# Kernel optimization log

Measured on AMD Instinct MI355X. Metric: run time of the kernel, lower is better.

Reference implementation:

```python
import jax, jax.numpy as jnp
import numpy as np

RNN = 2048
NZ = 64
IN = 69  # 54 dofs + 15 actions


def gru_cell(x, h, w_ih, w_hh, b_ih, b_hh):
    gi = x @ w_ih.T + b_ih
    gh = h @ w_hh.T + b_hh
    i_r, i_z, i_n = jnp.split(gi, 3, axis=-1)
    h_r, h_z, h_n = jnp.split(gh, 3, axis=-1)
    r = jax.nn.sigmoid(i_r + h_r)
    z = jax.nn.sigmoid(i_z + h_z)
    n = jnp.tanh(i_n + r * h_n)
    return (1.0 - z) * n + z * h


def setup_inputs() -> dict:
    key = jax.random.key(0)
    ks = jax.random.split(key, 24)
    s = 0.02
    d = {
        'encoder_inputs': jax.random.normal(ks[0], (256, 49, IN), jnp.float32),
        'decoder_inputs': jax.random.normal(ks[1], (256, 25, IN), jnp.float32),
        'eps': jax.random.normal(ks[2], (256, NZ), jnp.float32),
        'fc0_w': jax.random.normal(ks[3], (RNN, 2 * IN), jnp.float32) * s,
        'fc0_b': jnp.zeros((RNN,), jnp.float32),
        'fc1_w': jax.random.normal(ks[4], (RNN, NZ + IN), jnp.float32) * s,
        'fc1_b': jnp.zeros((RNN,), jnp.float32),
        'fc2_w': jax.random.normal(ks[5], (IN, RNN), jnp.float32) * s,
        'fc2_b': jnp.zeros((IN,), jnp.float32),
        'mu_w': jax.random.normal(ks[6], (NZ, RNN), jnp.float32) * s,
        'mu_b': jnp.zeros((NZ,), jnp.float32),
        'sigma_w': jax.random.normal(ks[7], (NZ, RNN), jnp.float32) * s,
        'sigma_b': jnp.zeros((NZ,), jnp.float32),
        'c1_wih': jax.random.normal(ks[8], (3 * RNN, RNN), jnp.float32) * s,
        'c1_whh': jax.random.normal(ks[9], (3 * RNN, RNN), jnp.float32) * s,
        'c1_bih': jnp.zeros((3 * RNN,), jnp.float32),
        'c1_bhh': jnp.zeros((3 * RNN,), jnp.float32),
        'c2_wih': jax.random.normal(ks[10], (3 * RNN, IN), jnp.float32) * s,
        'c2_whh': jax.random.normal(ks[11], (3 * RNN, RNN), jnp.float32) * s,
        'c2_bih': jnp.zeros((3 * RNN,), jnp.float32),
        'c2_bhh': jnp.zeros((3 * RNN,), jnp.float32),
    }
    return d


def reference(encoder_inputs, decoder_inputs, eps, fc0_w, fc0_b, fc1_w, fc1_b, fc2_w, fc2_b,
              mu_w, mu_b, sigma_w, sigma_b, c1_wih, c1_whh, c1_bih, c1_bhh,
              c2_wih, c2_whh, c2_bih, c2_bhh):
    B = encoder_inputs.shape[0]
    enc_t = jnp.transpose(encoder_inputs, (1, 0, 2))  # [S-1, B, IN]
    dec_t = jnp.transpose(decoder_inputs, (1, 0, 2))  # [T, B, IN]
    # encoder step inputs: cat(enc[i], enc[i+1]); last step pairs with dec[0]
    nxt = jnp.concatenate([enc_t[1:], dec_t[:1]], axis=0)
    pairs = jnp.concatenate([enc_t, nxt], axis=-1)  # [S-1, B, 2*IN]
    x = pairs @ fc0_w.T + fc0_b  # fc0, [S-1, B, RNN]
    # precompute input-to-hidden GEMMs for all encoder steps
    gi_all = x @ c1_wih.T + c1_bih  # [S-1, B, 3*RNN]

    def enc_step(h, gi):
        gh = h @ c1_whh.T + c1_bhh
        i_r, i_z, i_n = jnp.split(gi, 3, axis=-1)
        h_r, h_z, h_n = jnp.split(gh, 3, axis=-1)
        r = jax.nn.sigmoid(i_r + h_r)
        z = jax.nn.sigmoid(i_z + h_z)
        n = jnp.tanh(i_n + r * h_n)
        return (1.0 - z) * n + z * h, None

    h0 = jnp.zeros((B, RNN), encoder_inputs.dtype)
    state, _ = jax.lax.scan(enc_step, h0, gi_all)

    z_mu = state @ mu_w.T + mu_b
    z_logvar = state @ sigma_w.T + sigma_b
    z = z_mu + eps * jnp.exp(0.5 * z_logvar)

    dec0 = dec_t[0]  # [B, IN]
    state = jnp.concatenate([z, dec0], axis=-1) @ fc1_w.T + fc1_b

    def dec_step(carry, _):
        h, inp = carry
        h = gru_cell(inp, h, c2_wih, c2_whh, c2_bih, c2_bhh)
        out = inp + (h @ fc2_w.T + fc2_b)  # residual feedback (eval: no dropout)
        return (h, out), out

    T = dec_t.shape[0]
    _, ys = jax.lax.scan(dec_step, (state, dec0), None, length=T)  # [T, B, IN]
    outputs = jnp.transpose(ys, (1, 0, 2))
    return outputs, z_mu, z_logvar
```

## Files before the change

kernel.cpp:

```cpp
#include <hip/hip_runtime.h>
#include <stdint.h>

#define B_    256
#define SE    49
#define TD    25
#define INDIM 69
#define RNN   2048
#define NZ    64
#define G3    6144

typedef __attribute__((ext_vector_type(8))) short short8_t;
typedef __attribute__((ext_vector_type(4))) float f32x4;
typedef unsigned short u16;

__device__ __forceinline__ float b2f(u16 u) {
  union { unsigned u; float f; } c; c.u = ((unsigned)u) << 16; return c.f;
}
__device__ __forceinline__ u16 f2b(float f) {
  union { float f; unsigned u; } c; c.f = f;
  unsigned u = c.u;
  return (u16)((u + 0x7FFFu + ((u >> 16) & 1u)) >> 16);
}
__device__ __forceinline__ float sigm(float x) { return 1.f / (1.f + __expf(-x)); }

__device__ __forceinline__ int rmap(int R) {
  int bn = R / 96, rem = R % 96;
  int nw = rem / 48, g = (rem % 48) / 16, jj = rem % 16;
  return g * RNN + bn * 32 + nw * 16 + jj;
}

__global__ void k_reorder(const float* __restrict__ src, u16* __restrict__ dst, int K, int Kp) {
  int total = G3 * Kp;
  for (int i = blockIdx.x * blockDim.x + threadIdx.x; i < total; i += gridDim.x * blockDim.x) {
    int R = i / Kp, c = i % Kp;
    dst[i] = (c < K) ? f2b(src[(size_t)rmap(R) * K + c]) : (u16)0;
  }
}

__global__ void k_fc0T(const float* __restrict__ fc0w, u16* __restrict__ dst) {
  int total = 256 * RNN;
  for (int i = blockIdx.x * blockDim.x + threadIdx.x; i < total; i += gridDim.x * blockDim.x) {
    int r = i >> 11, k = i & (RNN - 1);
    dst[i] = (r < 2 * INDIM) ? f2b(fc0w[(size_t)k * (2 * INDIM) + r]) : (u16)0;
  }
}

__global__ void k_fc2T(const float* __restrict__ fc2w, u16* __restrict__ dst) {
  int total = 96 * RNN;
  for (int i = blockIdx.x * blockDim.x + threadIdx.x; i < total; i += gridDim.x * blockDim.x) {
    int r = i >> 11, k = i & (RNN - 1);
    dst[i] = (r < INDIM) ? f2b(fc2w[(size_t)r * RNN + k]) : (u16)0;
  }
}

__global__ void k_pairs(const float* __restrict__ enc, const float* __restrict__ dec,
                        u16* __restrict__ pairs) {
  int total = SE * B_ * 256;
  for (int i = blockIdx.x * blockDim.x + threadIdx.x; i < total; i += gridDim.x * blockDim.x) {
    int c = i & 255, rb = i >> 8;
    int b = rb & 255, t = rb >> 8;
    float v = 0.f;
    if (c < INDIM) v = enc[((size_t)b * SE + t) * INDIM + c];
    else if (c < 2 * INDIM) {
      int cc = c - INDIM;
      v = (t < SE - 1) ? enc[((size_t)b * SE + t + 1) * INDIM + cc]
                       : dec[(size_t)b * TD * INDIM + cc];
    }
    pairs[i] = f2b(v);
  }
}

__global__ void k_msT(const float* __restrict__ muw, const float* __restrict__ sgw,
                      float* __restrict__ dst) {
  int total = RNN * 128;
  for (int i = blockIdx.x * blockDim.x + threadIdx.x; i < total; i += gridDim.x * blockDim.x) {
    int k = i >> 7, n = i & 127;
    dst[i] = (n < NZ) ? muw[(size_t)n * RNN + k] : sgw[(size_t)(n - NZ) * RNN + k];
  }
}

__global__ void k_fc1T(const float* __restrict__ w, float* __restrict__ dst) {
  int total = (NZ + INDIM) * RNN;
  for (int i = blockIdx.x * blockDim.x + threadIdx.x; i < total; i += gridDim.x * blockDim.x) {
    int k = i >> 11, n = i & (RNN - 1);
    dst[i] = w[(size_t)n * (NZ + INDIM) + k];
  }
}

__global__ void k_bias(const float* __restrict__ c1wih, const float* __restrict__ fc0b,
                       const float* __restrict__ c1bih, const float* __restrict__ c1bhh,
                       const float* __restrict__ c2wih, const float* __restrict__ fc2b,
                       const float* __restrict__ c2bih, const float* __restrict__ c2bhh,
                       float* __restrict__ ebi, float* __restrict__ ebh,
                       float* __restrict__ dbi0, float* __restrict__ dbi1, float* __restrict__ dbh) {
  int R = blockIdx.x;
  int orig = rmap(R);
  float s = 0.f;
  for (int k = threadIdx.x; k < RNN; k += 256) s += c1wih[(size_t)orig * RNN + k] * fc0b[k];
  __shared__ float red[256];
  red[threadIdx.x] = s; __syncthreads();
  for (int st = 128; st > 0; st >>= 1) {
    if (threadIdx.x < st) red[threadIdx.x] += red[threadIdx.x + st];
    __syncthreads();
  }
  if (threadIdx.x == 0) {
    float k3 = 0.f;
    for (int o = 0; o < INDIM; ++o) k3 += c2wih[(size_t)orig * INDIM + o] * fc2b[o];
    ebi[R] = red[0] + c1bih[orig];
    ebh[R] = c1bhh[orig];
    float d0 = c2bih[orig];
    dbi0[R] = d0;
    dbi1[R] = d0 + k3;
    dbh[R] = c2bhh[orig];
  }
}

__global__ void k_init(float* __restrict__ hf, u16* __restrict__ hbf, float* __restrict__ fbuf,
                       float* __restrict__ omu, float* __restrict__ olv) {
  int i = blockIdx.x * blockDim.x + threadIdx.x;
  if (i < B_ * RNN) { hf[i] = 0.f; hbf[i] = 0; }
  if (i < 3 * B_ * 96) fbuf[i] = 0.f;
  if (i < B_ * NZ) { omu[i] = 0.f; olv[i] = 0.f; }
}

__global__ __launch_bounds__(256) void gemm_bt(
    const u16* __restrict__ A, const u16* __restrict__ W,
    u16* __restrict__ Cb, int N, int K)
{
  constexpr int BM = 128, BN = 128, BK = 64, LDK = BK + 8;
  __shared__ u16 sA[BM * LDK];
  __shared__ u16 sW[BN * LDK];
  const int ntn = N / BN;
  const int bm = blockIdx.x / ntn, bn = blockIdx.x % ntn;
  const int tid = threadIdx.x, lane = tid & 63, wave = tid >> 6;
  const int wr = wave >> 1, wc = wave & 1;
  f32x4 acc[4][4];
#pragma unroll
// ... 24 lines not shown
      for (int m = 0; m < 4; ++m)
#pragma unroll
        for (int n = 0; n < 4; ++n)
          acc[m][n] = __builtin_amdgcn_mfma_f32_16x16x32_bf16(fa[m], fb[n], acc[m][n], 0, 0, 0);
    }
    __syncthreads();
  }
  const int crow = (lane >> 4) * 4, ccol = lane & 15;
#pragma unroll
  for (int n = 0; n < 4; ++n) {
    int col = bn * BN + wc * 64 + n * 16 + ccol;
#pragma unroll
    for (int m = 0; m < 4; ++m)
#pragma unroll
      for (int r = 0; r < 4; ++r) {
        int rowi = bm * BM + wr * 64 + m * 16 + crow + r;
        Cb[(size_t)rowi * N + col] = f2b(acc[m][n][r]);
      }
  }
}

struct Args {
  const u16 *pairs, *Wenc, *whh1, *whh2, *wih2, *fc2T;
  const float *ebi, *ebh, *dbi0, *dbi1, *dbh;
  const float *eps, *dec, *fc1_b, *fc2_b;
  const float *mswT, *fc1T, *mu_b, *sg_b;
  float* hf;
  u16*   hbf;
  float* fbuf;
  float* inp;
  u16*   inpbf;
  float* fc1x;
  float *out, *out_mu, *out_lv;
};

__device__ __forceinline__ void stage_gh(short8_t (&ra)[4], short8_t (&rw)[6],
    const u16* __restrict__ A, const u16* __restrict__ W,
    int rowA0, int rowW0, int k0, int tid) {
#pragma unroll
  for (int p = 0; p < 4; ++p) {
    int s = tid + p * 512, r = s >> 5, c = s & 31;
    ra[p] = *(const short8_t*)&A[(size_t)(rowA0 + r) * RNN + k0 + c * 8];
  }
#pragma unroll
  for (int p = 0; p < 6; ++p) {
    int s = tid + p * 512, r = s >> 5, c = s & 31;
    rw[p] = *(const short8_t*)&W[(size_t)(rowW0 + r) * RNN + k0 + c * 8];
  }
}

__device__ __forceinline__ void write_AW(char* sA, char* sW,
    short8_t (&ra)[4], short8_t (&rw)[6], int tid) {
#pragma unroll
  for (int p = 0; p < 4; ++p) {
    int s = tid + p * 512, r = s >> 5, c = s & 31;
    *(short8_t*)&sA[r * 512 + ((c ^ ((r & 7) << 2)) * 16)] = ra[p];
  }
#pragma unroll
  for (int p = 0; p < 6; ++p) {
    int s = tid + p * 512, r = s >> 5, c = s & 31;
    *(short8_t*)&sW[r * 512 + ((c ^ ((r & 7) << 2)) * 16)] = rw[p];
  }
}

__device__ __forceinline__ void compute2(const char* sA, const char* sW,
    f32x4 (&aR)[4], f32x4 (&aZ)[4], f32x4 (&aN)[4], int kg, int nw, int lane) {
#pragma unroll
  for (int s = 0; s < 2; ++s) {
    const int L = kg * 8 + s * 4 + (lane >> 4);
    short8_t fa[4], fbv[3];
#pragma unroll
    for (int m = 0; m < 4; ++m) {
      int r = m * 16 + (lane & 15);
      fa[m] = *(const short8_t*)&sA[r * 512 + ((L ^ ((r & 7) << 2)) * 16)];
    }
#pragma unroll
    for (int g = 0; g < 3; ++g) {
      int r = nw * 48 + g * 16 + (lane & 15);
      fbv[g] = *(const short8_t*)&sW[r * 512 + ((L ^ ((r & 7) << 2)) * 16)];
    }
#pragma unroll
    for (int m = 0; m < 4; ++m) {
      aR[m] = __builtin_amdgcn_mfma_f32_16x16x32_bf16(fa[m], fbv[0], aR[m], 0, 0, 0);
      aZ[m] = __builtin_amdgcn_mfma_f32_16x16x32_bf16(fa[m], fbv[1], aZ[m], 0, 0, 0);
      aN[m] = __builtin_amdgcn_mfma_f32_16x16x32_bf16(fa[m], fbv[2], aN[m], 0, 0, 0);
    }
  }
}

__device__ __forceinline__ void reduce_and_gate(
    f32x4 (&aR)[4], f32x4 (&aZ)[4], f32x4 (&aNI)[4], f32x4 (&aNH)[4],
    char* smem, int tid, int bm, int bn,
    const float* __restrict__ bi, const float* __restrict__ bh,
    const float* __restrict__ hfold, float* __restrict__ hfnew, u16* __restrict__ hbnew) {
  const int lane = tid & 63, wid = tid >> 6;
  auto wr16 = [&](int slots, int w) {
#pragma unroll
    for (int m = 0; m < 4; ++m) {
      *(f32x4*)&smem[(((0 * 4 + m) * slots + w) * 64 + lane) * 16] = aR[m];
      *(f32x4*)&smem[(((1 * 4 + m) * slots + w) * 64 + lane) * 16] = aZ[m];
      *(f32x4*)&smem[(((2 * 4 + m) * slots + w) * 64 + lane) * 16] = aNI[m];
      *(f32x4*)&smem[(((3 * 4 + m) * slots + w) * 64 + lane) * 16] = aNH[m];
    }
  };
  auto add16 = [&](int slots, int w) {
#pragma unroll
    for (int m = 0; m < 4; ++m) {
      aR[m]  += *(const f32x4*)&smem[(((0 * 4 + m) * slots + w) * 64 + lane) * 16];
      aZ[m]  += *(const f32x4*)&smem[(((1 * 4 + m) * slots + w) * 64 + lane) * 16];
      aNI[m] += *(const f32x4*)&smem[(((2 * 4 + m) * slots + w) * 64 + lane) * 16];
      aNH[m] += *(const f32x4*)&smem[(((3 * 4 + m) * slots + w) * 64 + lane) * 16];
// ... 10 lines not shown
    add16(2, wid);
    const int nw = wid, jj = lane & 15;
    const int Rb = bn * 96 + nw * 48;
    const float biR = bi[Rb + jj],      bhR = bh[Rb + jj];
    const float biZ = bi[Rb + 16 + jj], bhZ = bh[Rb + 16 + jj];
    const float biN = bi[Rb + 32 + jj], bhN = bh[Rb + 32 + jj];
    const int j = bn * 32 + nw * 16 + jj;
#pragma unroll
    for (int m = 0; m < 4; ++m)
#pragma unroll
      for (int q = 0; q < 4; ++q) {
        int b = bm * 64 + m * 16 + ((lane >> 4) << 2) + q;
        float r = sigm(aR[m][q] + biR + bhR);
        float z = sigm(aZ[m][q] + biZ + bhZ);
        float nn = 2.f * sigm(2.f * ((aNI[m][q] + biN) + r * (aNH[m][q] + bhN))) - 1.f;
        float hv = (1.f - z) * nn + z * hfold[(size_t)b * RNN + j];
        hfnew[(size_t)b * RNN + j] = hv;
        hbnew[(size_t)b * RNN + j] = f2b(hv);
      }
  }
}

__global__ __launch_bounds__(512, 1) void k_enc(Args a, int t) {
  __shared__ char smem[81920];
  char* sA = smem;
  char* sW = smem + 32768;
  const int tid = threadIdx.x, lane = tid & 63, wid = tid >> 6;
  const int kg = wid >> 1, nw = wid & 1;
  const int bm = blockIdx.x >> 6, bn = blockIdx.x & 63;
  const int rowA0 = bm * 64, rowW0 = bn * 96;
  const int pin = t & 1, pout = pin ^ 1;
  const u16* hin = a.hbf + (size_t)pin * B_ * RNN;
  const float* hfold = a.hf + (size_t)pin * B_ * RNN;
  float* hfnew = a.hf + (size_t)pout * B_ * RNN;
  u16* hbnew = a.hbf + (size_t)pout * B_ * RNN;

  f32x4 aR[4], aZ[4], aNI[4], aNH[4];
#pragma unroll
  for (int m = 0; m < 4; ++m) {
    aR[m] = (f32x4)(0.f); aZ[m] = (f32x4)(0.f);
    aNI[m] = (f32x4)(0.f); aNH[m] = (f32x4)(0.f);
  }

  short8_t ra[4], rw[6], ra2[4], rw2[6];
  const u16* P = a.pairs + (size_t)t * B_ * 256;
#pragma unroll
  for (int p = 0; p < 4; ++p) {
    int s = tid + p * 512, r = s >> 5, c = s & 31;
    ra[p] = *(const short8_t*)&P[(size_t)(rowA0 + r) * 256 + c * 8];
  }
#pragma unroll
  for (int p = 0; p < 6; ++p) {
    int s = tid + p * 512, r = s >> 5, c = s & 31;
    rw[p] = *(const short8_t*)&a.Wenc[(size_t)(rowW0 + r) * 256 + c * 8];
  }
  write_AW(sA, sW, ra, rw, tid);
  stage_gh(ra2, rw2, hin, a.whh1, rowA0, rowW0, 0, tid);
  __syncthreads();
  compute2(sA, sW, aR, aZ, aNI, kg, nw, lane);
  for (int i = 1; i <= 8; ++i) {
#pragma unroll
    for (int q = 0; q < 4; ++q) ra[q] = ra2[q];
#pragma unroll
    for (int q = 0; q < 6; ++q) rw[q] = rw2[q];
    __syncthreads();
    write_AW(sA, sW, ra, rw, tid);
    if (i < 8) stage_gh(ra2, rw2, hin, a.whh1, rowA0, rowW0, i * 256, tid);
    __syncthreads();
    compute2(sA, sW, aR, aZ, aNH, kg, nw, lane);
  }
  reduce_and_gate(aR, aZ, aNI, aNH, smem, tid, bm, bn, a.ebi, a.ebh, hfold, hfnew, hbnew);
}

__global__ __launch_bounds__(512, 1) void k_dec(Args a, int t) {
  __shared__ char smem[81920];
  char* sA = smem;
  char* sW = smem + 32768;
  const int tid = threadIdx.x, lane = tid & 63, wid = tid >> 6;
  const int kg = wid >> 1, nw = wid & 1;
  const int bm = blockIdx.x >> 6, bn = blockIdx.x & 63;
  const int rowA0 = bm * 64, rowW0 = bn * 96;
  const int pin = t & 1, pout = pin ^ 1;
  const int irs = (t + 1) & 1, iws = t & 1;
  const int frd = (t + 2) % 3;
  const u16* hin = a.hbf + (size_t)pin * B_ * RNN;
  const float* hfold = a.hf + (size_t)pin * B_ * RNN;
  float* hfnew = a.hf + (size_t)pout * B_ * RNN;
  u16* hbnew = a.hbf + (size_t)pout * B_ * RNN;
  const int gtid = blockIdx.x * 512 + tid;

  if (t >= 1 && gtid < B_ * INDIM) {
    int b = gtid / INDIM, o = gtid % INDIM;
    float v = a.inp[(size_t)irs * B_ * INDIM + gtid] +
              a.fbuf[(size_t)frd * B_ * 96 + b * 96 + o] + a.fc2_b[o];
    a.out[((size_t)b * TD + (t - 1)) * INDIM + o] = v;
    a.inp[(size_t)iws * B_ * INDIM + gtid] = v;
    a.inpbf[(size_t)iws * B_ * 128 + b * 128 + o] = f2b(v);
  }
  if (gtid < B_ * 96)
    a.fbuf[(size_t)((t + 1) % 3) * B_ * 96 + gtid] = 0.f;

  f32x4 aR[4], aZ[4], aNI[4], aNH[4];
#pragma unroll
  for (int m = 0; m < 4; ++m) {
    aR[m] = (f32x4)(0.f); aZ[m] = (f32x4)(0.f);
    aNI[m] = (f32x4)(0.f); aNH[m] = (f32x4)(0.f);
  }

  short8_t ra[4], rw[6], ra2[4], rw2[6];
  const u16* inpA = a.inpbf + (size_t)irs * B_ * 128;
  const float* F = a.fbuf + (size_t)frd * B_ * 96;
#pragma unroll
  for (int p = 0; p < 4; ++p) {
    int s = tid + p * 512, r = s >> 5, c = s & 31;
    if (c < 16) {
      ra[p] = *(const short8_t*)&inpA[(size_t)(rowA0 + r) * 128 + c * 8];
    } else {
      short8_t v;
#pragma unroll
      for (int e = 0; e < 8; ++e) {
        int o = (c - 16) * 8 + e;
        float fv = (o < 96) ? F[(size_t)(rowA0 + r) * 96 + o] : 0.f;
        v[e] = (short)f2b(fv);
      }
      ra[p] = v;
    }
  }
#pragma unroll
  for (int p = 0; p < 6; ++p) {
    int s = tid + p * 512, r = s >> 5, c = s & 31;
    rw[p] = *(const short8_t*)&a.wih2[(size_t)(rowW0 + r) * 128 + (c & 15) * 8];
  }
  __syncthreads();
  write_AW(sA, sW, ra, rw, tid);
  stage_gh(ra2, rw2, hin, a.whh2, rowA0, rowW0, 0, tid);
  __syncthreads();
  compute2(sA, sW, aR, aZ, aNI, kg, nw, lane);
  for (int i = 1; i <= 8; ++i) {
#pragma unroll
    for (int q = 0; q < 4; ++q) ra[q] = ra2[q];
#pragma unroll
    for (int q = 0; q < 6; ++q) rw[q] = rw2[q];
    __syncthreads();
    write_AW(sA, sW, ra, rw, tid);
    if (i < 8) stage_gh(ra2, rw2, hin, a.whh2, rowA0, rowW0, i * 256, tid);
    __syncthreads();
    compute2(sA, sW, aR, aZ, aNH, kg, nw, lane);
  }
  reduce_and_gate(aR, aZ, aNI, aNH, smem, tid, bm, bn,
                  (t >= 1) ? a.dbi1 : a.dbi0, a.dbh, hfold, hfnew, hbnew);

  __syncthreads();
  if (tid < 256) {
    int r = tid >> 2, c16 = tid & 3;
    *(short8_t*)&smem[r * 80 + c16 * 16] =
        *(const short8_t*)&hbnew[(size_t)(bm * 64 + r) * RNN + bn * 32 + c16 * 8];
  }
  if (tid < 384) {
    int r = tid >> 2, c16 = tid & 3;
    if (tid < 256) {
    }
    (void)r; (void)c16;
  }
  {
    int s2 = tid;
    if (s2 < 384) {
      int r = s2 >> 2, c16 = s2 & 3;
      *(short8_t*)&smem[5120 + r * 80 + c16 * 16] =
          *(const short8_t*)&a.fc2T[(size_t)r * RNN + bn * 32 + c16 * 8];
    }
  }
  __syncthreads();
  if (wid < 4) {
    const int wr = wid >> 1, wc = wid & 1;
    short8_t fa[2], fb[3];
    f32x4 accf[2][3];
#pragma unroll
    for (int m = 0; m < 2; ++m)
#pragma unroll
      for (int n = 0; n < 3; ++n) accf[m][n] = (f32x4)(0.f);
#pragma unroll
    for (int m = 0; m < 2; ++m) {
      int r = wr * 32 + m * 16 + (lane & 15);
      fa[m] = *(const short8_t*)&smem[r * 80 + ((lane >> 4) << 4)];
    }
#pragma unroll
    for (int n = 0; n < 3; ++n) {
      int r = wc * 48 + n * 16 + (lane & 15);
      fb[n] = *(const short8_t*)&smem[5120 + r * 80 + ((lane >> 4) << 4)];
    }
#pragma unroll
    for (int m = 0; m < 2; ++m)
#pragma unroll
      for (int n = 0; n < 3; ++n)
        accf[m][n] = __builtin_amdgcn_mfma_f32_16x16x32_bf16(fa[m], fb[n], accf[m][n], 0, 0, 0);
    float* fdst = a.fbuf + (size_t)(t % 3) * B_ * 96;
#pragma unroll
    for (int m = 0; m < 2; ++m)
#pragma unroll
      for (int n = 0; n < 3; ++n)
#pragma unroll
        for (int q = 0; q < 4; ++q) {
          int row = bm * 64 + wr * 32 + m * 16 + ((lane >> 4) << 2) + q;
          int col = wc * 48 + n * 16 + (lane & 15);
          atomicAdd(&fdst[row * 96 + col], accf[m][n][q]);
        }
  }
}

__global__ __launch_bounds__(256) void k_ms(Args a) {
  __shared__ float hs[16 * 128];
  const int bt = blockIdx.x >> 4, kc = blockIdx.x & 15;
  const int tid = threadIdx.x;
  const float* h1 = a.hf + (size_t)B_ * RNN;
#pragma unroll
  for (int p = 0; p < 8; ++p) {
    int ii = tid + p * 256;
    int bl = ii >> 7, kl = ii & 127;
    hs[ii] = h1[(size_t)(bt * 16 + bl) * RNN + kc * 128 + kl];
  }
  __syncthreads();
  const int n = tid & 127, bg = tid >> 7;
  const float* wp = a.mswT + (size_t)(kc * 128) * 128 + n;
  float ps[8];
#pragma unroll
  for (int i = 0; i < 8; ++i) ps[i] = 0.f;
  for (int k = 0; k < 128; ++k) {
    float wv = wp[(size_t)k * 128];
#pragma unroll
    for (int i = 0; i < 8; ++i) ps[i] += wv * hs[(bg * 8 + i) * 128 + k];
  }
#pragma unroll
  for (int i = 0; i < 8; ++i) {
    int b = bt * 16 + bg * 8 + i;
    if (n < NZ) atomicAdd(&a.out_mu[b * NZ + n], ps[i]);
    else        atomicAdd(&a.out_lv[b * NZ + (n - NZ)], ps[i]);
  }
}

__global__ void k_sample(Args a) {
  int gid = blockIdx.x * blockDim.x + threadIdx.x;
  if (gid < B_ * NZ) {
    int b = gid >> 6, n = gid & 63;
    float mu = a.out_mu[gid] + a.mu_b[n];
    float lv = a.out_lv[gid] + a.sg_b[n];
    a.out_mu[gid] = mu;
    a.out_lv[gid] = lv;
    a.fc1x[b * 144 + n] = mu + a.eps[gid] * __expf(0.5f * lv);
  }
  if (gid < B_ * 128) {
    int b = gid >> 7, c = gid & 127;
    float v = (c < INDIM) ? a.dec[(size_t)b * TD * INDIM + c] : 0.f;
    u16 vb = f2b(v);
    a.inpbf[(size_t)b * 128 + c] = vb;
    a.inpbf[(size_t)B_ * 128 + b * 128 + c] = vb;
    if (c < INDIM) {
      a.inp[b * INDIM + c] = v;
      a.inp[B_ * INDIM + b * INDIM + c] = v;
      a.fc1x[b * 144 + NZ + c] = v;
    }
  }
}

__global__ __launch_bounds__(256) void k_fc1(Args a) {
  __shared__ float xs[16 * 144];
  const int bt = blockIdx.x >> 3, nt = blockIdx.x & 7;
  const int tid = threadIdx.x;
#pragma unroll
  for (int p = 0; p < 9; ++p) {
    int ii = tid + p * 256;
    if (ii < 16 * 144) {
      int bl = ii / 144, k = ii % 144;
      xs[ii] = (k < NZ + INDIM) ? a.fc1x[(size_t)(bt * 16 + bl) * 144 + k] : 0.f;
    }
  }
  __syncthreads();
  const int n = nt * 256 + tid;
  float s[16];
#pragma unroll
  for (int i = 0; i < 16; ++i) s[i] = 0.f;
  for (int k = 0; k < NZ + INDIM; ++k) {
    float wv = a.fc1T[(size_t)k * RNN + n];
#pragma unroll
    for (int i = 0; i < 16; ++i) s[i] += wv * xs[i * 144 + k];
  }
  float bv = a.fc1_b[n];
#pragma unroll
  for (int i = 0; i < 16; ++i) {
    int b = bt * 16 + i;
    float v = s[i] + bv;
    a.hf[(size_t)b * RNN + n] = v;
    a.hbf[(size_t)b * RNN + n] = f2b(v);
  }
}

__global__ void k_tail(Args a) {
  int i = blockIdx.x * blockDim.x + threadIdx.x;
  if (i < B_ * INDIM) {
    int b = i / INDIM, o = i % INDIM;
    float v = a.inp[(size_t)(24 & 1) * B_ * INDIM + i] +
              a.fbuf[(size_t)(24 % 3) * B_ * 96 + b * 96 + o] + a.fc2_b[o];
    a.out[((size_t)b * TD + 24) * INDIM + o] = v;
  }
}

extern "C" void kernel_launch(void* const* d_in, const int* in_sizes, int n_in,
                              void* d_out, int out_size, void* d_ws, size_t ws_size,
                              hipStream_t stream)
{
  const float* enc    = (const float*)d_in[0];
  const float* dec    = (const float*)d_in[1];
  const float* eps    = (const float*)d_in[2];
  const float* fc0_w  = (const float*)d_in[3];
  const float* fc0_b  = (const float*)d_in[4];
  const float* fc1_w  = (const float*)d_in[5];
// ... 11 lines not shown
  const float* c2_wih = (const float*)d_in[17];
  const float* c2_whh = (const float*)d_in[18];
  const float* c2_bih = (const float*)d_in[19];
  const float* c2_bhh = (const float*)d_in[20];

  float* out_outputs = (float*)d_out;
  float* out_mu = out_outputs + (size_t)B_ * TD * INDIM;
  float* out_lv = out_mu + (size_t)B_ * NZ;

  char* ws = (char*)d_ws;
  size_t off = 0;
  auto alloc = [&](size_t bytes) -> void* {
    void* p = ws + off; off += (bytes + 255) & ~(size_t)255; return p;
  };

  u16* whh1_r = (u16*)alloc((size_t)G3 * RNN * 2);
  u16* whh2_r = (u16*)alloc((size_t)G3 * RNN * 2);
  u16* wih1_r = (u16*)alloc((size_t)G3 * RNN * 2);
  u16* wih2_r = (u16*)alloc((size_t)G3 * 128 * 2);
  u16* fc0T   = (u16*)alloc((size_t)256 * RNN * 2);
  u16* fc2T   = (u16*)alloc((size_t)96 * RNN * 2);
  u16* Wenc   = (u16*)alloc((size_t)G3 * 256 * 2);
  u16* pairs  = (u16*)alloc((size_t)SE * B_ * 256 * 2);
  float* hf   = (float*)alloc((size_t)2 * B_ * RNN * 4);
  u16* hbf    = (u16*)alloc((size_t)2 * B_ * RNN * 2);
  float* fbuf = (float*)alloc((size_t)3 * B_ * 96 * 4);
  float* inp  = (float*)alloc((size_t)2 * B_ * INDIM * 4);
  u16* inpbf  = (u16*)alloc((size_t)2 * B_ * 128 * 2);
  float* fc1x = (float*)alloc((size_t)B_ * 144 * 4);
  float* mswT = (float*)alloc((size_t)RNN * 128 * 4);
  float* fc1T = (float*)alloc((size_t)(NZ + INDIM) * RNN * 4);
  float* ebi  = (float*)alloc((size_t)G3 * 4);
  float* ebh  = (float*)alloc((size_t)G3 * 4);
  float* dbi0 = (float*)alloc((size_t)G3 * 4);
  float* dbi1 = (float*)alloc((size_t)G3 * 4);
  float* dbh  = (float*)alloc((size_t)G3 * 4);
  (void)ws_size; (void)in_sizes; (void)n_in; (void)out_size;

  k_reorder<<<4096, 256, 0, stream>>>(c1_whh, whh1_r, RNN, RNN);
  k_reorder<<<4096, 256, 0, stream>>>(c2_whh, whh2_r, RNN, RNN);
  k_reorder<<<4096, 256, 0, stream>>>(c1_wih, wih1_r, RNN, RNN);
  k_reorder<<<1024, 256, 0, stream>>>(c2_wih, wih2_r, INDIM, 128);
  k_fc0T<<<512, 256, 0, stream>>>(fc0_w, fc0T);
  k_fc2T<<<256, 256, 0, stream>>>(fc2_w, fc2T);
  k_pairs<<<2048, 256, 0, stream>>>(enc, dec, pairs);
  k_msT<<<256, 256, 0, stream>>>(mu_w, sg_w, mswT);
  k_fc1T<<<256, 256, 0, stream>>>(fc1_w, fc1T);
  k_bias<<<G3, 256, 0, stream>>>(c1_wih, fc0_b, c1_bih, c1_bhh,
                                 c2_wih, fc2_b, c2_bih, c2_bhh,
                                 ebi, ebh, dbi0, dbi1, dbh);

  Args a;
  a.pairs = pairs; a.Wenc = Wenc; a.whh1 = whh1_r; a.whh2 = whh2_r;
  a.wih2 = wih2_r; a.fc2T = fc2T;
  a.ebi = ebi; a.ebh = ebh; a.dbi0 = dbi0; a.dbi1 = dbi1; a.dbh = dbh;
  a.eps = eps; a.dec = dec; a.fc1_b = fc1_b; a.fc2_b = fc2_b;
  a.mswT = mswT; a.fc1T = fc1T; a.mu_b = mu_b; a.sg_b = sg_b;
  a.hf = hf; a.hbf = hbf; a.fbuf = fbuf; a.inp = inp; a.inpbf = inpbf;
  a.fc1x = fc1x; a.out = out_outputs; a.out_mu = out_mu; a.out_lv = out_lv;

  k_init<<<2048, 256, 0, stream>>>(hf, hbf, fbuf, out_mu, out_lv);
  gemm_bt<<<(G3 / 128) * (256 / 128), 256, 0, stream>>>(wih1_r, fc0T, Wenc, 256, RNN);

  for (int t = 0; t < SE; ++t)
    k_enc<<<256, 512, 0, stream>>>(a, t);
  k_ms<<<256, 256, 0, stream>>>(a);
  k_sample<<<128, 256, 0, stream>>>(a);
  k_fc1<<<128, 256, 0, stream>>>(a);
  for (int t = 0; t < TD; ++t)
    k_dec<<<256, 512, 0, stream>>>(a, t);
  k_tail<<<69, 256, 0, stream>>>(a);
}
```

Baseline: 1.737 ms.

## Load MFMA fragments directly from global memory and convert small projections to bf16 MFMA

The encoder and decoder step kernels stop staging A/W tiles through LDS with a double-buffered register pipeline and load MFMA fragments straight from global memory. Blocks are remapped so the four batch tiles sharing a weight slice run as adjacent block IDs, which favours cache reuse of the weight rows. The mu/sigma and fc1 projections become bf16 MFMA kernels, the fc0 bias is folded into the encoder GEMM through a constant-one input column, and k_bias drops its reduction. This removes LDS traffic and barriers, but it relies on L2/MALL caching for reuse, and computing mu/logvar in bf16 from the bf16 hidden state loses some precision.

```diff
diff --git a/kernel.cpp b/kernel.cpp
--- a/kernel.cpp
+++ b/kernel.cpp
@@ -13,15 +13,15 @@
 typedef __attribute__((ext_vector_type(4))) float f32x4;
 typedef unsigned short u16;
 
-__device__ __forceinline__ float b2f(u16 u) {
-  union { unsigned u; float f; } c; c.u = ((unsigned)u) << 16; return c.f;
-}
 __device__ __forceinline__ u16 f2b(float f) {
   union { float f; unsigned u; } c; c.f = f;
   unsigned u = c.u;
   return (u16)((u + 0x7FFFu + ((u >> 16) & 1u)) >> 16);
 }
 __device__ __forceinline__ float sigm(float x) { return 1.f / (1.f + __expf(-x)); }
+__device__ __forceinline__ short8_t ldbf(const u16* __restrict__ p, size_t off) {
+  return *(const short8_t*)&p[off];
+}
 
 __device__ __forceinline__ int rmap(int R) {
   int bn = R / 96, rem = R % 96;
@@ -37,11 +37,15 @@
   }
 }
 
-__global__ void k_fc0T(const float* __restrict__ fc0w, u16* __restrict__ dst) {
+__global__ void k_fc0T(const float* __restrict__ fc0w, const float* __restrict__ fc0b,
+                       u16* __restrict__ dst) {
   int total = 256 * RNN;
   for (int i = blockIdx.x * blockDim.x + threadIdx.x; i < total; i += gridDim.x * blockDim.x) {
     int r = i >> 11, k = i & (RNN - 1);
-    dst[i] = (r < 2 * INDIM) ? f2b(fc0w[(size_t)k * (2 * INDIM) + r]) : (u16)0;
+    float v = 0.f;
+    if (r < 2 * INDIM) v = fc0w[(size_t)k * (2 * INDIM) + r];
+    else if (r == 2 * INDIM) v = fc0b[k];
+    dst[i] = f2b(v);
   }
 }
 
@@ -65,54 +69,44 @@
       int cc = c - INDIM;
       v = (t < SE - 1) ? enc[((size_t)b * SE + t + 1) * INDIM + cc]
                        : dec[(size_t)b * TD * INDIM + cc];
-    }
+    } else if (c == 2 * INDIM) v = 1.0f;
     pairs[i] = f2b(v);
   }
 }
 
-__global__ void k_msT(const float* __restrict__ muw, const float* __restrict__ sgw,
-                      float* __restrict__ dst) {
-  int total = RNN * 128;
+__global__ void k_msB(const float* __restrict__ muw, const float* __restrict__ sgw,
+                      u16* __restrict__ dst) {
+  int total = 128 * RNN;
   for (int i = blockIdx.x * blockDim.x + threadIdx.x; i < total; i += gridDim.x * blockDim.x) {
-    int k = i >> 7, n = i & 127;
-    dst[i] = (n < NZ) ? muw[(size_t)n * RNN + k] : sgw[(size_t)(n - NZ) * RNN + k];
-  }
-}
-
-__global__ void k_fc1T(const float* __restrict__ w, float* __restrict__ dst) {
-  int total = (NZ + INDIM) * RNN;
+    int n = i >> 11, k = i & (RNN - 1);
+    dst[i] = (n < NZ) ? f2b(muw[(size_t)n * RNN + k]) : f2b(sgw[(size_t)(n - NZ) * RNN + k]);
+  }
+}
+
+__global__ void k_fc1B(const float* __restrict__ w, u16* __restrict__ dst) {
+  int total = RNN * 192;
   for (int i = blockIdx.x * blockDim.x + threadIdx.x; i < total; i += gridDim.x * blockDim.x) {
-    int k = i >> 11, n = i & (RNN - 1);
-    dst[i] = w[(size_t)n * (NZ + INDIM) + k];
-  }
-}
-
-__global__ void k_bias(const float* __restrict__ c1wih, const float* __restrict__ fc0b,
-                       const float* __restrict__ c1bih, const float* __restrict__ c1bhh,
+    int n = i / 192, k = i % 192;
+    dst[i] = (k < NZ + INDIM) ? f2b(w[(size_t)n * (NZ + INDIM) + k]) : (u16)0;
+  }
+}
+
+__global__ void k_bias(const float* __restrict__ c1bih, const float* __restrict__ c1bhh,
                        const float* __restrict__ c2wih, const float* __restrict__ fc2b,
                        const float* __restrict__ c2bih, const float* __restrict__ c2bhh,
                        float* __restrict__ ebi, float* __restrict__ ebh,
                        float* __restrict__ dbi0, float* __restrict__ dbi1, float* __restrict__ dbh) {
-  int R = blockIdx.x;
+  int R = blockIdx.x * blockDim.x + threadIdx.x;
+  if (R >= G3) return;
   int orig = rmap(R);
-  float s = 0.f;
-  for (int k = threadIdx.x; k < RNN; k += 256) s += c1wih[(size_t)orig * RNN + k] * fc0b[k];
-  __shared__ float red[256];
-  red[threadIdx.x] = s; __syncthreads();
-  for (int st = 128; st > 0; st >>= 1) {
-    if (threadIdx.x < st) red[threadIdx.x] += red[threadIdx.x + st];
-    __syncthreads();
-  }
-  if (threadIdx.x == 0) {
-    float k3 = 0.f;
-    for (int o = 0; o < INDIM; ++o) k3 += c2wih[(size_t)orig * INDIM + o] * fc2b[o];
-    ebi[R] = red[0] + c1bih[orig];
-    ebh[R] = c1bhh[orig];
-    float d0 = c2bih[orig];
-    dbi0[R] = d0;
-    dbi1[R] = d0 + k3;
-    dbh[R] = c2bhh[orig];
-  }
+  float k3 = 0.f;
+  for (int o = 0; o < INDIM; ++o) k3 += c2wih[(size_t)orig * INDIM + o] * fc2b[o];
+  ebi[R] = c1bih[orig];
+  ebh[R] = c1bhh[orig];
+  float d0 = c2bih[orig];
+  dbi0[R] = d0;
+  dbi1[R] = d0 + k3;
+  dbh[R] = c2bhh[orig];
 }
 
 __global__ void k_init(float* __restrict__ hf, u16* __restrict__ hbf, float* __restrict__ fbuf,
@@ -183,71 +177,17 @@
 
 struct Args {
   const u16 *pairs, *Wenc, *whh1, *whh2, *wih2, *fc2T;
+  const u16 *msB, *fc1wB;
   const float *ebi, *ebh, *dbi0, *dbi1, *dbh;
-  const float *eps, *dec, *fc1_b, *fc2_b;
-  const float *mswT, *fc1T, *mu_b, *sg_b;
+  const float *eps, *dec, *fc1_b, *fc2_b, *mu_b, *sg_b;
   float* hf;
   u16*   hbf;
   float* fbuf;
   float* inp;
   u16*   inpbf;
-  float* fc1x;
+  u16*   fc1xB;
   float *out, *out_mu, *out_lv;
 };
-
-__device__ __forceinline__ void stage_gh(short8_t (&ra)[4], short8_t (&rw)[6],
-    const u16* __restrict__ A, const u16* __restrict__ W,
-    int rowA0, int rowW0, int k0, int tid) {
-#pragma unroll
-  for (int p = 0; p < 4; ++p) {
-    int s = tid + p * 512, r = s >> 5, c = s & 31;
-    ra[p] = *(const short8_t*)&A[(size_t)(rowA0 + r) * RNN + k0 + c * 8];
-  }
-#pragma unroll
-  for (int p = 0; p < 6; ++p) {
-    int s = tid + p * 512, r = s >> 5, c = s & 31;
-    rw[p] = *(const short8_t*)&W[(size_t)(rowW0 + r) * RNN + k0 + c * 8];
-  }
-}
-
-__device__ __forceinline__ void write_AW(char* sA, char* sW,
-    short8_t (&ra)[4], short8_t (&rw)[6], int tid) {
-#pragma unroll
-  for (int p = 0; p < 4; ++p) {
-    int s = tid + p * 512, r = s >> 5, c = s & 31;
-    *(short8_t*)&sA[r * 512 + ((c ^ ((r & 7) << 2)) * 16)] = ra[p];
-  }
-#pragma unroll
-  for (int p = 0; p < 6; ++p) {
-    int s = tid + p * 512, r = s >> 5, c = s & 31;
-    *(short8_t*)&sW[r * 512 + ((c ^ ((r & 7) << 2)) * 16)] = rw[p];
-  }
-}
-
-__device__ __forceinline__ void compute2(const char* sA, const char* sW,
-    f32x4 (&aR)[4], f32x4 (&aZ)[4], f32x4 (&aN)[4], int kg, int nw, int lane) {
-#pragma unroll
-  for (int s = 0; s < 2; ++s) {
-    const int L = kg * 8 + s * 4 + (lane >> 4);
-    short8_t fa[4], fbv[3];
-#pragma unroll
-    for (int m = 0; m < 4; ++m) {
-      int r = m * 16 + (lane & 15);
-      fa[m] = *(const short8_t*)&sA[r * 512 + ((L ^ ((r & 7) << 2)) * 16)];
-    }
-#pragma unroll
-    for (int g = 0; g < 3; ++g) {
-      int r = nw * 48 + g * 16 + (lane & 15);
-      fbv[g] = *(const short8_t*)&sW[r * 512 + ((L ^ ((r & 7) << 2)) * 16)];
-    }
-#pragma unroll
-    for (int m = 0; m < 4; ++m) {
-      aR[m] = __builtin_amdgcn_mfma_f32_16x16x32_bf16(fa[m], fbv[0], aR[m], 0, 0, 0);
-      aZ[m] = __builtin_amdgcn_mfma_f32_16x16x32_bf16(fa[m], fbv[1], aZ[m], 0, 0, 0);
-      aN[m] = __builtin_amdgcn_mfma_f32_16x16x32_bf16(fa[m], fbv[2], aN[m], 0, 0, 0);
-    }
-  }
-}
 
 __device__ __forceinline__ void reduce_and_gate(
     f32x4 (&aR)[4], f32x4 (&aZ)[4], f32x4 (&aNI)[4], f32x4 (&aNH)[4],
@@ -304,13 +244,14 @@
 }
 
 __global__ __launch_bounds__(512, 1) void k_enc(Args a, int t) {
-  __shared__ char smem[81920];
-  char* sA = smem;
-  char* sW = smem + 32768;
+  __shared__ char smem[65536];
   const int tid = threadIdx.x, lane = tid & 63, wid = tid >> 6;
   const int kg = wid >> 1, nw = wid & 1;
-  const int bm = blockIdx.x >> 6, bn = blockIdx.x & 63;
-  const int rowA0 = bm * 64, rowW0 = bn * 96;
+  const int bid = blockIdx.x;
+  const int bm = (bid >> 3) & 3;
+  const int bn = (bid & 7) | ((bid >> 5) << 3);
+  const int rowA0 = bm * 64, rowW0 = bn * 96 + nw * 48;
+  const int fr = lane & 15, fq = (lane >> 4) << 3;
   const int pin = t & 1, pout = pin ^ 1;
   const u16* hin = a.hbf + (size_t)pin * B_ * RNN;
   const float* hfold = a.hf + (size_t)pin * B_ * RNN;
@@ -324,44 +265,50 @@
     aNI[m] = (f32x4)(0.f); aNH[m] = (f32x4)(0.f);
   }
 
-  short8_t ra[4], rw[6], ra2[4], rw2[6];
   const u16* P = a.pairs + (size_t)t * B_ * 256;
 #pragma unroll
-  for (int p = 0; p < 4; ++p) {
-    int s = tid + p * 512, r = s >> 5, c = s & 31;
-    ra[p] = *(const short8_t*)&P[(size_t)(rowA0 + r) * 256 + c * 8];
-  }
-#pragma unroll
-  for (int p = 0; p < 6; ++p) {
-    int s = tid + p * 512, r = s >> 5, c = s & 31;
-    rw[p] = *(const short8_t*)&a.Wenc[(size_t)(rowW0 + r) * 256 + c * 8];
-  }
-  write_AW(sA, sW, ra, rw, tid);
-  stage_gh(ra2, rw2, hin, a.whh1, rowA0, rowW0, 0, tid);
-  __syncthreads();
-  compute2(sA, sW, aR, aZ, aNI, kg, nw, lane);
-  for (int i = 1; i <= 8; ++i) {
-#pragma unroll
-    for (int q = 0; q < 4; ++q) ra[q] = ra2[q];
-#pragma unroll
-    for (int q = 0; q < 6; ++q) rw[q] = rw2[q];
-    __syncthreads();
-    write_AW(sA, sW, ra, rw, tid);
-    if (i < 8) stage_gh(ra2, rw2, hin, a.whh1, rowA0, rowW0, i * 256, tid);
-    __syncthreads();
-    compute2(sA, sW, aR, aZ, aNH, kg, nw, lane);
+  for (int ks = 0; ks < 2; ++ks) {
+    const int k = kg * 64 + ks * 32 + fq;
+    short8_t fa[4], fb[3];
+#pragma unroll
+    for (int m = 0; m < 4; ++m) fa[m] = ldbf(P, (size_t)(rowA0 + m * 16 + fr) * 256 + k);
+#pragma unroll
+    for (int g = 0; g < 3; ++g) fb[g] = ldbf(a.Wenc, (size_t)(rowW0 + g * 16 + fr) * 256 + k);
+#pragma unroll
+    for (int m = 0; m < 4; ++m) {
+      aR[m]  = __builtin_amdgcn_mfma_f32_16x16x32_bf16(fa[m], fb[0], aR[m], 0, 0, 0);
+      aZ[m]  = __builtin_amdgcn_mfma_f32_16x16x32_bf16(fa[m], fb[1], aZ[m], 0, 0, 0);
+      aNI[m] = __builtin_amdgcn_mfma_f32_16x16x32_bf16(fa[m], fb[2], aNI[m], 0, 0, 0);
+    }
+  }
+  const int kb = kg * 512;
+#pragma unroll 4
+  for (int ks = 0; ks < 16; ++ks) {
+    const int k = kb + ks * 32 + fq;
+    short8_t fa[4], fb[3];
+#pragma unroll
+    for (int m = 0; m < 4; ++m) fa[m] = ldbf(hin, (size_t)(rowA0 + m * 16 + fr) * RNN + k);
+#pragma unroll
+    for (int g = 0; g < 3; ++g) fb[g] = ldbf(a.whh1, (size_t)(rowW0 + g * 16 + fr) * RNN + k);
+#pragma unroll
+    for (int m = 0; m < 4; ++m) {
+      aR[m]  = __builtin_amdgcn_mfma_f32_16x16x32_bf16(fa[m], fb[0], aR[m], 0, 0, 0);
+      aZ[m]  = __builtin_amdgcn_mfma_f32_16x16x32_bf16(fa[m], fb[1], aZ[m], 0, 0, 0);
+      aNH[m] = __builtin_amdgcn_mfma_f32_16x16x32_bf16(fa[m], fb[2], aNH[m], 0, 0, 0);
+    }
   }
   reduce_and_gate(aR, aZ, aNI, aNH, smem, tid, bm, bn, a.ebi, a.ebh, hfold, hfnew, hbnew);
 }
 
 __global__ __launch_bounds__(512, 1) void k_dec(Args a, int t) {
-  __shared__ char smem[81920];
-  char* sA = smem;
-  char* sW = smem + 32768;
+  __shared__ char smem[65536];
   const int tid = threadIdx.x, lane = tid & 63, wid = tid >> 6;
   const int kg = wid >> 1, nw = wid & 1;
-  const int bm = blockIdx.x >> 6, bn = blockIdx.x & 63;
-  const int rowA0 = bm * 64, rowW0 = bn * 96;
+  const int bid = blockIdx.x;
+  const int bm = (bid >> 3) & 3;
+  const int bn = (bid & 7) | ((bid >> 5) << 3);
+  const int rowA0 = bm * 64, rowW0 = bn * 96 + nw * 48;
+  const int fr = lane & 15, fq = (lane >> 4) << 3;
   const int pin = t & 1, pout = pin ^ 1;
   const int irs = (t + 1) & 1, iws = t & 1;
   const int frd = (t + 2) % 3;
@@ -369,7 +316,7 @@
   const float* hfold = a.hf + (size_t)pin * B_ * RNN;
   float* hfnew = a.hf + (size_t)pout * B_ * RNN;
   u16* hbnew = a.hbf + (size_t)pout * B_ * RNN;
-  const int gtid = blockIdx.x * 512 + tid;
+  const int gtid = bid * 512 + tid;
 
   if (t >= 1 && gtid < B_ * INDIM) {
     int b = gtid / INDIM, o = gtid % INDIM;
@@ -389,88 +336,87 @@
     aNI[m] = (f32x4)(0.f); aNH[m] = (f32x4)(0.f);
   }
 
-  short8_t ra[4], rw[6], ra2[4], rw2[6];
-  const u16* inpA = a.inpbf + (size_t)irs * B_ * 128;
-  const float* F = a.fbuf + (size_t)frd * B_ * 96;
-#pragma unroll
-  for (int p = 0; p < 4; ++p) {
-    int s = tid + p * 512, r = s >> 5, c = s & 31;
-    if (c < 16) {
-      ra[p] = *(const short8_t*)&inpA[(size_t)(rowA0 + r) * 128 + c * 8];
-    } else {
-      short8_t v;
-#pragma unroll
-      for (int e = 0; e < 8; ++e) {
-        int o = (c - 16) * 8 + e;
-        float fv = (o < 96) ? F[(size_t)(rowA0 + r) * 96 + o] : 0.f;
-        v[e] = (short)f2b(fv);
+  if (kg < 2) {
+    const u16* inpA = a.inpbf + (size_t)irs * B_ * 128;
+#pragma unroll
+    for (int ks = 0; ks < 2; ++ks) {
+      const int k = kg * 64 + ks * 32 + fq;
+      short8_t fa[4], fb[3];
+#pragma unroll
+      for (int m = 0; m < 4; ++m) fa[m] = ldbf(inpA, (size_t)(rowA0 + m * 16 + fr) * 128 + k);
+#pragma unroll
+      for (int g = 0; g < 3; ++g) fb[g] = ldbf(a.wih2, (size_t)(rowW0 + g * 16 + fr) * 128 + k);
+#pragma unroll
+      for (int m = 0; m < 4; ++m) {
+        aR[m]  = __builtin_amdgcn_mfma_f32_16x16x32_bf16(fa[m], fb[0], aR[m], 0, 0, 0);
+        aZ[m]  = __builtin_amdgcn_mfma_f32_16x16x32_bf16(fa[m], fb[1], aZ[m], 0, 0, 0);
+        aNI[m] = __builtin_amdgcn_mfma_f32_16x16x32_bf16(fa[m], fb[2], aNI[m], 0, 0, 0);
       }
-      ra[p] = v;
-    }
-  }
-#pragma unroll
-  for (int p = 0; p < 6; ++p) {
-    int s = tid + p * 512, r = s >> 5, c = s & 31;
-    rw[p] = *(const short8_t*)&a.wih2[(size_t)(rowW0 + r) * 128 + (c & 15) * 8];
-  }
-  __syncthreads();
-  write_AW(sA, sW, ra, rw, tid);
-  stage_gh(ra2, rw2, hin, a.whh2, rowA0, rowW0, 0, tid);
-  __syncthreads();
-  compute2(sA, sW, aR, aZ, aNI, kg, nw, lane);
-  for (int i = 1; i <= 8; ++i) {
-#pragma unroll
-    for (int q = 0; q < 4; ++q) ra[q] = ra2[q];
-#pragma unroll
-    for (int q = 0; q < 6; ++q) rw[q] = rw2[q];
-    __syncthreads();
-    write_AW(sA, sW, ra, rw, tid);
-    if (i < 8) stage_gh(ra2, rw2, hin, a.whh2, rowA0, rowW0, i * 256, tid);
-    __syncthreads();
-    compute2(sA, sW, aR, aZ, aNH, kg, nw, lane);
+    }
+  } else {
+    const float* F = a.fbuf + (size_t)frd * B_ * 96;
+#pragma unroll
+    for (int ks = 0; ks < 2; ++ks) {
+      if (kg == 3 && ks == 1) continue;
+      const int kw = (kg - 2) * 64 + ks * 32 + fq;
+      short8_t fa[4], fb[3];
+#pragma unroll
+      for (int m = 0; m < 4; ++m) {
+        const int rrow = rowA0 + m * 16 + fr;
+        f32x4 v0 = *(const f32x4*)&F[(size_t)rrow * 96 + kw];
+        f32x4 v1 = *(const f32x4*)&F[(size_t)rrow * 96 + kw + 4];
+        short8_t v;
+        v[0] = (short)f2b(v0[0]); v[1] = (short)f2b(v0[1]);
+        v[2] = (short)f2b(v0[2]); v[3] = (short)f2b(v0[3]);
+        v[4] = (short)f2b(v1[0]); v[5] = (short)f2b(v1[1]);
+        v[6] = (short)f2b(v1[2]); v[7] = (short)f2b(v1[3]);
+        fa[m] = v;
+      }
+#pragma unroll
+      for (int g = 0; g < 3; ++g) fb[g] = ldbf(a.wih2, (size_t)(rowW0 + g * 16 + fr) * 128 + kw);
+#pragma unroll
+      for (int m = 0; m < 4; ++m) {
+        aR[m]  = __builtin_amdgcn_mfma_f32_16x16x32_bf16(fa[m], fb[0], aR[m], 0, 0, 0);
+        aZ[m]  = __builtin_amdgcn_mfma_f32_16x16x32_bf16(fa[m], fb[1], aZ[m], 0, 0, 0);
+        aNI[m] = __builtin_amdgcn_mfma_f32_16x16x32_bf16(fa[m], fb[2], aNI[m], 0, 0, 0);
+      }
+    }
+  }
+  const int kb = kg * 512;
+#pragma unroll 4
+  for (int ks = 0; ks < 16; ++ks) {
+    const int k = kb + ks * 32 + fq;
+    short8_t fa[4], fb[3];
+#pragma unroll
+    for (int m = 0; m < 4; ++m) fa[m] = ldbf(hin, (size_t)(rowA0 + m * 16 + fr) * RNN + k);
+#pragma unroll
+    for (int g = 0; g < 3; ++g) fb[g] = ldbf(a.whh2, (size_t)(rowW0 + g * 16 + fr) * RNN + k);
+#pragma unroll
+    for (int m = 0; m < 4; ++m) {
+      aR[m]  = __builtin_amdgcn_mfma_f32_16x16x32_bf16(fa[m], fb[0], aR[m], 0, 0, 0);
+      aZ[m]  = __builtin_amdgcn_mfma_f32_16x16x32_bf16(fa[m], fb[1], aZ[m], 0, 0, 0);
+      aNH[m] = __builtin_amdgcn_mfma_f32_16x16x32_bf16(fa[m], fb[2], aNH[m], 0, 0, 0);
+    }
   }
   reduce_and_gate(aR, aZ, aNI, aNH, smem, tid, bm, bn,
                   (t >= 1) ? a.dbi1 : a.dbi0, a.dbh, hfold, hfnew, hbnew);
 
-  __syncthreads();
-  if (tid < 256) {
-    int r = tid >> 2, c16 = tid & 3;
-    *(short8_t*)&smem[r * 80 + c16 * 16] =
-        *(const short8_t*)&hbnew[(size_t)(bm * 64 + r) * RNN + bn * 32 + c16 * 8];
-  }
-  if (tid < 384) {
-    int r = tid >> 2, c16 = tid & 3;
-    if (tid < 256) {
-    }
-    (void)r; (void)c16;
-  }
-  {
-    int s2 = tid;
-    if (s2 < 384) {
-      int r = s2 >> 2, c16 = s2 & 3;
-      *(short8_t*)&smem[5120 + r * 80 + c16 * 16] =
-          *(const short8_t*)&a.fc2T[(size_t)r * RNN + bn * 32 + c16 * 8];
-    }
-  }
   __syncthreads();
   if (wid < 4) {
     const int wr = wid >> 1, wc = wid & 1;
+    const int kcol = bn * 32 + fq;
     short8_t fa[2], fb[3];
+#pragma unroll
+    for (int m = 0; m < 2; ++m)
+      fa[m] = ldbf(hbnew, (size_t)(bm * 64 + wr * 32 + m * 16 + fr) * RNN + kcol);
+#pragma unroll
+    for (int n = 0; n < 3; ++n)
+      fb[n] = ldbf(a.fc2T, (size_t)(wc * 48 + n * 16 + fr) * RNN + kcol);
     f32x4 accf[2][3];
 #pragma unroll
     for (int m = 0; m < 2; ++m)
 #pragma unroll
       for (int n = 0; n < 3; ++n) accf[m][n] = (f32x4)(0.f);
-#pragma unroll
-    for (int m = 0; m < 2; ++m) {
-      int r = wr * 32 + m * 16 + (lane & 15);
-      fa[m] = *(const short8_t*)&smem[r * 80 + ((lane >> 4) << 4)];
-    }
-#pragma unroll
-    for (int n = 0; n < 3; ++n) {
-      int r = wc * 48 + n * 16 + (lane & 15);
-      fb[n] = *(const short8_t*)&smem[5120 + r * 80 + ((lane >> 4) << 4)];
-    }
 #pragma unroll
     for (int m = 0; m < 2; ++m)
 #pragma unroll
@@ -490,34 +436,44 @@
   }
 }
 
-__global__ __launch_bounds__(256) void k_ms(Args a) {
-  __shared__ float hs[16 * 128];
-  const int bt = blockIdx.x >> 4, kc = blockIdx.x & 15;
-  const int tid = threadIdx.x;
-  const float* h1 = a.hf + (size_t)B_ * RNN;
-#pragma unroll
-  for (int p = 0; p < 8; ++p) {
-    int ii = tid + p * 256;
-    int bl = ii >> 7, kl = ii & 127;
-    hs[ii] = h1[(size_t)(bt * 16 + bl) * RNN + kc * 128 + kl];
-  }
-  __syncthreads();
-  const int n = tid & 127, bg = tid >> 7;
-  const float* wp = a.mswT + (size_t)(kc * 128) * 128 + n;
-  float ps[8];
-#pragma unroll
-  for (int i = 0; i < 8; ++i) ps[i] = 0.f;
-  for (int k = 0; k < 128; ++k) {
-    float wv = wp[(size_t)k * 128];
-#pragma unroll
-    for (int i = 0; i < 8; ++i) ps[i] += wv * hs[(bg * 8 + i) * 128 + k];
-  }
-#pragma unroll
-  for (int i = 0; i < 8; ++i) {
-    int b = bt * 16 + bg * 8 + i;
-    if (n < NZ) atomicAdd(&a.out_mu[b * NZ + n], ps[i]);
-    else        atomicAdd(&a.out_lv[b * NZ + (n - NZ)], ps[i]);
-  }
+__global__ __launch_bounds__(256) void k_msm(Args a) {
+  const int bm = blockIdx.x >> 3, kc = blockIdx.x & 7;
+  const int lane = threadIdx.x & 63, wid = threadIdx.x >> 6;
+  const int wr = wid >> 1, wc = wid & 1;
+  const int fr = lane & 15, fq = (lane >> 4) << 3;
+  const u16* h1 = a.hbf + (size_t)B_ * RNN;
+  f32x4 acc[4][4];
+#pragma unroll
+  for (int m = 0; m < 4; ++m)
+#pragma unroll
+    for (int n = 0; n < 4; ++n) acc[m][n] = (f32x4)(0.f);
+#pragma unroll
+  for (int ks = 0; ks < 8; ++ks) {
+    const int k = kc * 256 + ks * 32 + fq;
+    short8_t fa[4], fb[4];
+#pragma unroll
+    for (int m = 0; m < 4; ++m)
+      fa[m] = ldbf(h1, (size_t)(bm * 128 + wr * 64 + m * 16 + fr) * RNN + k);
+#pragma unroll
+    for (int n = 0; n < 4; ++n)
+      fb[n] = ldbf(a.msB, (size_t)(wc * 64 + n * 16 + fr) * RNN + k);
+#pragma unroll
+    for (int m = 0; m < 4; ++m)
+#pragma unroll
+      for (int n = 0; n < 4; ++n)
+        acc[m][n] = __builtin_amdgcn_mfma_f32_16x16x32_bf16(fa[m], fb[n], acc[m][n], 0, 0, 0);
+  }
+#pragma unroll
+  for (int m = 0; m < 4; ++m)
+#pragma unroll
+    for (int n = 0; n < 4; ++n)
+#pragma unroll
+      for (int q = 0; q < 4; ++q) {
+        int row = bm * 128 + wr * 64 + m * 16 + ((lane >> 4) << 2) + q;
+        int col = wc * 64 + n * 16 + (lane & 15);
+        if (col < NZ) atomicAdd(&a.out_mu[row * NZ + col], acc[m][n][q]);
+        else          atomicAdd(&a.out_lv[row * NZ + col - NZ], acc[m][n][q]);
+      }
 }
 
 __global__ void k_sample(Args a) {
@@ -528,7 +484,7 @@
     float lv = a.out_lv[gid] + a.sg_b[n];
     a.out_mu[gid] = mu;
     a.out_lv[gid] = lv;
-    a.fc1x[b * 144 + n] = mu + a.eps[gid] * __expf(0.5f * lv);
+    a.fc1xB[b * 192 + n] = f2b(mu + a.eps[gid] * __expf(0.5f * lv));
   }
   if (gid < B_ * 128) {
     int b = gid >> 7, c = gid & 127;
@@ -539,40 +495,54 @@
     if (c < INDIM) {
       a.inp[b * INDIM + c] = v;
       a.inp[B_ * INDIM + b * INDIM + c] = v;
-      a.fc1x[b * 144 + NZ + c] = v;
-    }
-  }
-}
-
-__global__ __launch_bounds__(256) void k_fc1(Args a) {
-  __shared__ float xs[16 * 144];
-  const int bt = blockIdx.x >> 3, nt = blockIdx.x & 7;
-  const int tid = threadIdx.x;
-#pragma unroll
-  for (int p = 0; p < 9; ++p) {
-    int ii = tid + p * 256;
-    if (ii < 16 * 144) {
-      int bl = ii / 144, k = ii % 144;
-      xs[ii] = (k < NZ + INDIM) ? a.fc1x[(size_t)(bt * 16 + bl) * 144 + k] : 0.f;
-    }
-  }
-  __syncthreads();
-  const int n = nt * 256 + tid;
-  float s[16];
-#pragma unroll
-  for (int i = 0; i < 16; ++i) s[i] = 0.f;
-  for (int k = 0; k < NZ + INDIM; ++k) {
-    float wv = a.fc1T[(size_t)k * RNN + n];
-#pragma unroll
-    for (int i = 0; i < 16; ++i) s[i] += wv * xs[i * 144 + k];
-  }
-  float bv = a.fc1_b[n];
-#pragma unroll
-  for (int i = 0; i < 16; ++i) {
-    int b = bt * 16 + i;
-    float v = s[i] + bv;
-    a.hf[(size_t)b * RNN + n] = v;
-    a.hbf[(size_t)b * RNN + n] = f2b(v);
+      a.fc1xB[b * 192 + NZ + c] = f2b(v);
+    }
+  }
+  if (gid < B_ * 192) {
+    int c = gid % 192;
+    if (c >= NZ + INDIM) a.fc1xB[gid] = 0;
+  }
+}
+
+__global__ __launch_bounds__(256) void k_fc1m(Args a) {
+  const int bm = blockIdx.x >> 4, bn = blockIdx.x & 15;
+  const int lane = threadIdx.x & 63, wid = threadIdx.x >> 6;
+  const int wr = wid >> 1, wc = wid & 1;
+  const int fr = lane & 15, fq = (lane >> 4) << 3;
+  f32x4 acc[4][4];
+#pragma unroll
+  for (int m = 0; m < 4; ++m)
+#pragma unroll
+    for (int n = 0; n < 4; ++n) acc[m][n] = (f32x4)(0.f);
+#pragma unroll
+  for (int ks = 0; ks < 6; ++ks) {
+    const int k = ks * 32 + fq;
+    short8_t fa[4], fb[4];
+#pragma unroll
+    for (int m = 0; m < 4; ++m)
+      fa[m] = ldbf(a.fc1xB, (size_t)(bm * 128 + wr * 64 + m * 16 + fr) * 192 + k);
+#pragma unroll
+    for (int n = 0; n < 4; ++n)
+      fb[n] = ldbf(a.fc1wB, (size_t)(bn * 128 + wc * 64 + n * 16 + fr) * 192 + k);
+#pragma unroll
+    for (int m = 0; m < 4; ++m)
+#pragma unroll
+      for (int n = 0; n < 4; ++n)
+        acc[m][n] = __builtin_amdgcn_mfma_f32_16x16x32_bf16(fa[m], fb[n], acc[m][n], 0, 0, 0);
+  }
+#pragma unroll
+  for (int n = 0; n < 4; ++n) {
+    const int col = bn * 128 + wc * 64 + n * 16 + (lane & 15);
+    const float bv = a.fc1_b[col];
+#pragma unroll
+    for (int m = 0; m < 4; ++m)
+#pragma unroll
+      for (int q = 0; q < 4; ++q) {
+        int row = bm * 128 + wr * 64 + m * 16 + ((lane >> 4) << 2) + q;
+        float v = acc[m][n][q] + bv;
+        a.hf[(size_t)row * RNN + col] = v;
+        a.hbf[(size_t)row * RNN + col] = f2b(v);
+      }
   }
 }
 
@@ -630,14 +600,14 @@
   u16* fc2T   = (u16*)alloc((size_t)96 * RNN * 2);
   u16* Wenc   = (u16*)alloc((size_t)G3 * 256 * 2);
   u16* pairs  = (u16*)alloc((size_t)SE * B_ * 256 * 2);
+  u16* msB    = (u16*)alloc((size_t)128 * RNN * 2);
+  u16* fc1wB  = (u16*)alloc((size_t)RNN * 192 * 2);
   float* hf   = (float*)alloc((size_t)2 * B_ * RNN * 4);
   u16* hbf    = (u16*)alloc((size_t)2 * B_ * RNN * 2);
   float* fbuf = (float*)alloc((size_t)3 * B_ * 96 * 4);
   float* inp  = (float*)alloc((size_t)2 * B_ * INDIM * 4);
   u16* inpbf  = (u16*)alloc((size_t)2 * B_ * 128 * 2);
-  float* fc1x = (float*)alloc((size_t)B_ * 144 * 4);
-  float* mswT = (float*)alloc((size_t)RNN * 128 * 4);
-  float* fc1T = (float*)alloc((size_t)(NZ + INDIM) * RNN * 4);
+  u16* fc1xB  = (u16*)alloc((size_t)B_ * 192 * 2);
   float* ebi  = (float*)alloc((size_t)G3 * 4);
   float* ebh  = (float*)alloc((size_t)G3 * 4);
   float* dbi0 = (float*)alloc((size_t)G3 * 4);
@@ -649,32 +619,31 @@
   k_reorder<<<4096, 256, 0, stream>>>(c2_whh, whh2_r, RNN, RNN);
   k_reorder<<<4096, 256, 0, stream>>>(c1_wih, wih1_r, RNN, RNN);
   k_reorder<<<1024, 256, 0, stream>>>(c2_wih, wih2_r, INDIM, 128);
-  k_fc0T<<<512, 256, 0, stream>>>(fc0_w, fc0T);
+  k_fc0T<<<512, 256, 0, stream>>>(fc0_w, fc0_b, fc0T);
   k_fc2T<<<256, 256, 0, stream>>>(fc2_w, fc2T);
   k_pairs<<<2048, 256, 0, stream>>>(enc, dec, pairs);
-  k_msT<<<256, 256, 0, stream>>>(mu_w, sg_w, mswT);
-  k_fc1T<<<256, 256, 0, stream>>>(fc1_w, fc1T);
-  k_bias<<<G3, 256, 0, stream>>>(c1_wih, fc0_b, c1_bih, c1_bhh,
-                                 c2_wih, fc2_b, c2_bih, c2_bhh,
+  k_msB<<<256, 256, 0, stream>>>(mu_w, sg_w, msB);
+  k_fc1B<<<256, 256, 0, stream>>>(fc1_w, fc1wB);
+  k_bias<<<24, 256, 0, stream>>>(c1_bih, c1_bhh, c2_wih, fc2_b, c2_bih, c2_bhh,
                                  ebi, ebh, dbi0, dbi1, dbh);
 
   Args a;
   a.pairs = pairs; a.Wenc = Wenc; a.whh1 = whh1_r; a.whh2 = whh2_r;
-  a.wih2 = wih2_r; a.fc2T = fc2T;
+  a.wih2 = wih2_r; a.fc2T = fc2T; a.msB = msB; a.fc1wB = fc1wB;
   a.ebi = ebi; a.ebh = ebh; a.dbi0 = dbi0; a.dbi1 = dbi1; a.dbh = dbh;
   a.eps = eps; a.dec = dec; a.fc1_b = fc1_b; a.fc2_b = fc2_b;
-  a.mswT = mswT; a.fc1T = fc1T; a.mu_b = mu_b; a.sg_b = sg_b;
+  a.mu_b = mu_b; a.sg_b = sg_b;
   a.hf = hf; a.hbf = hbf; a.fbuf = fbuf; a.inp = inp; a.inpbf = inpbf;
-  a.fc1x = fc1x; a.out = out_outputs; a.out_mu = out_mu; a.out_lv = out_lv;
+  a.fc1xB = fc1xB; a.out = out_outputs; a.out_mu = out_mu; a.out_lv = out_lv;
 
   k_init<<<2048, 256, 0, stream>>>(hf, hbf, fbuf, out_mu, out_lv);
   gemm_bt<<<(G3 / 128) * (256 / 128), 256, 0, stream>>>(wih1_r, fc0T, Wenc, 256, RNN);
 
   for (int t = 0; t < SE; ++t)
     k_enc<<<256, 512, 0, stream>>>(a, t);
-  k_ms<<<256, 256, 0, stream>>>(a);
-  k_sample<<<128, 256, 0, stream>>>(a);
-  k_fc1<<<128, 256, 0, stream>>>(a);
+  k_msm<<<16, 256, 0, stream>>>(a);
+  k_sample<<<192, 256, 0, stream>>>(a);
+  k_fc1m<<<32, 256, 0, stream>>>(a);
   for (int t = 0; t < TD; ++t)
     k_dec<<<256, 512, 0, stream>>>(a, t);
   k_tail<<<69, 256, 0, stream>>>(a);
```

Result: slower. 2.769 ms (+59.4%).
